# Kernel tuning notes

Hardware: AMD Instinct MI355X
Metric: run time of the kernel (lower is better)

Reference implementation:

```python
import jax, jax.numpy as jnp
import numpy as np

N_NODES = 50000
N_EDGES = 800000
IN_DIM = 256
HID = 64
HEADS = 4
N_CLASSES = 40
NEG_SLOPE = 0.2  # DGL GATConv default LeakyReLU slope


def setup_inputs() -> dict:
    key = jax.random.key(0)
    ks = jax.random.split(key, 8)
    features = jax.random.normal(ks[0], (N_NODES, IN_DIM), dtype=jnp.float32)
    src = jax.random.randint(ks[1], (N_EDGES,), 0, N_NODES, dtype=jnp.int32)
    dst = jax.random.randint(ks[2], (N_EDGES,), 0, N_NODES, dtype=jnp.int32)
    # GATConv params (Xavier-ish scale)
    W0 = jax.random.normal(ks[3], (IN_DIM, HEADS * HID), dtype=jnp.float32) / np.sqrt(IN_DIM)
    attn_l = jax.random.normal(ks[4], (HEADS, HID), dtype=jnp.float32) / np.sqrt(HID)
    attn_r = jax.random.normal(ks[5], (HEADS, HID), dtype=jnp.float32) / np.sqrt(HID)
    # Final FC layer
    fc_W = jax.random.normal(ks[6], (HEADS * HID, N_CLASSES), dtype=jnp.float32) / np.sqrt(HEADS * HID)
    fc_b = jax.random.normal(ks[7], (N_CLASSES,), dtype=jnp.float32) * 0.01
    return {"features": features, "W0": W0, "attn_l": attn_l, "attn_r": attn_r,
            "fc_W": fc_W, "fc_b": fc_b, "src": src, "dst": dst}


def _gat_conv(feat, W, a_l, a_r, src, dst):
    # feat: [N, F_in] -> projected [N, H, D]
    h = (feat @ W).reshape(feat.shape[0], HEADS, HID)
    el = jnp.einsum('nhd,hd->nh', h, a_l)  # [N, H]
    er = jnp.einsum('nhd,hd->nh', h, a_r)  # [N, H]
    e = el[src] + er[dst]                  # [E, H]
    e = jnp.where(e > 0, e, NEG_SLOPE * e)  # LeakyReLU
    # segment softmax over incoming edges of each destination node
    m = jax.ops.segment_max(e, dst, num_segments=N_NODES)  # [N, H]
    m = jnp.where(jnp.isfinite(m), m, 0.0)
    ex = jnp.exp(e - m[dst])
    s = jax.ops.segment_sum(ex, dst, num_segments=N_NODES)  # [N, H]
    alpha = ex / s[dst]                                      # [E, H]
    # weighted aggregation of source features
    msgs = alpha[:, :, None] * h[src]                        # [E, H, D]
    return jax.ops.segment_sum(msgs, dst, num_segments=N_NODES)  # [N, H, D]


def reference(features, W0, attn_l, attn_r, fc_W, fc_b, src, dst):
    h = _gat_conv(features, W0, attn_l, attn_r, src, dst)   # [N, H, D]
    h = jax.nn.relu(h).reshape(N_NODES, HEADS * HID)        # flatten(1)
    # dropout is identity in eval mode (training=False)
    return h @ fc_W + fc_b                                  # [N, num_classes]
```

## Files before the change

kernel.cpp:

```cpp
#include <hip/hip_runtime.h>

#define N_NODES 50000
#define N_EDGES 800000
#define IN_DIM 256
#define HID 64
#define HEADS 4
#define NFEAT 256
#define N_CLASSES 40
#define NC_PAD 48
#define NEG_SLOPE 0.2f
#define BIN_CAP 64

typedef __attribute__((ext_vector_type(8))) short short8;
typedef __attribute__((ext_vector_type(4))) float f32x4;

__device__ __forceinline__ unsigned short f2bf(float x) {
    unsigned u = __float_as_uint(x);
    unsigned r = u + 0x7FFFu + ((u >> 16) & 1u);
    return (unsigned short)(r >> 16);
}
__device__ __forceinline__ float bf2f(unsigned short u) {
    return __uint_as_float(((unsigned)u) << 16);
}
__device__ __forceinline__ float bf_lo(unsigned u) {
    return __uint_as_float(u << 16);
}
__device__ __forceinline__ float bf_hi(unsigned u) {
    return __uint_as_float(u & 0xFFFF0000u);
}

__global__ __launch_bounds__(256) void pack_weights(
    const float* __restrict__ W0, unsigned short* __restrict__ Wf,
    const float* __restrict__ W2, unsigned short* __restrict__ Wf2,
    int* __restrict__ cnt)
{
    int t = blockIdx.x * 256 + threadIdx.x;
    if (t < N_NODES) cnt[t] = 0;
    if (t < 65536) {
        int c = t & 255;
        int k = t >> 8;
        int kb = k >> 5, r = k & 31;
        int g = r >> 3, e = r & 7;
        Wf[((size_t)(kb * 256 + c) * 4 + g) * 8 + e] = f2bf(W0[(size_t)k * 256 + c]);
    } else {
        int t2 = t - 65536;
        if (t2 >= 8 * NC_PAD * 32) return;
        int c = (t2 >> 5) % NC_PAD;
        int kb = t2 / (NC_PAD * 32);
        int r = t2 & 31;
        int g = r >> 3, e = r & 7;
        int k = kb * 32 + g * 8 + e;
        float v = (c < N_CLASSES) ? W2[(size_t)k * N_CLASSES + c] : 0.f;
        Wf2[((size_t)(kb * NC_PAD + c) * 4 + g) * 8 + e] = f2bf(v);
    }
}

__global__ __launch_bounds__(256) void proj_mfma(
    const float* __restrict__ feat, const unsigned short* __restrict__ Wf,
    const float* __restrict__ al, const float* __restrict__ ar,
    unsigned short* __restrict__ hb16, float* __restrict__ el, float* __restrict__ er)
{
    const int tid  = threadIdx.x;
    const int lane = tid & 63;
    const int w    = tid >> 6;
    const int c    = lane & 15;
    const int g    = lane >> 4;
    const int row0 = blockIdx.x * 64;

    float alv[16], arv[16];
    #pragma unroll
    for (int f = 0; f < 16; ++f) { alv[f] = al[f * 16 + c]; arv[f] = ar[f * 16 + c]; }

    f32x4 acc[16];
    #pragma unroll
    for (int f = 0; f < 16; ++f) acc[f] = (f32x4){0.f, 0.f, 0.f, 0.f};

    const int arow = min(row0 + w * 16 + c, N_NODES - 1);
    const float* ap = &feat[(size_t)arow * IN_DIM + g * 8];

    for (int kb = 0; kb < 8; ++kb) {
        float4 v0 = *reinterpret_cast<const float4*>(ap + kb * 32);
        float4 v1 = *reinterpret_cast<const float4*>(ap + kb * 32 + 4);
        unsigned short us[8];
        us[0]=f2bf(v0.x); us[1]=f2bf(v0.y); us[2]=f2bf(v0.z); us[3]=f2bf(v0.w);
        us[4]=f2bf(v1.x); us[5]=f2bf(v1.y); us[6]=f2bf(v1.z); us[7]=f2bf(v1.w);
        short8 av = *reinterpret_cast<short8*>(us);
        #pragma unroll
        for (int f = 0; f < 16; ++f) {
            short8 bv = *reinterpret_cast<const short8*>(
                &Wf[((size_t)(kb * 256 + f * 16 + c) * 4 + g) * 8]);
            acc[f] = __builtin_amdgcn_mfma_f32_16x16x32_bf16(av, bv, acc[f], 0, 0, 0);
        }
    }

    const int baserow = row0 + w * 16 + g * 4;
    #pragma unroll
    for (int reg = 0; reg < 4; ++reg) {
        int grow = baserow + reg;
        bool ok = grow < N_NODES;
        float pl[4] = {0.f,0.f,0.f,0.f}, pr[4] = {0.f,0.f,0.f,0.f};
        #pragma unroll
        for (int f = 0; f < 16; ++f) {
            float v = acc[f][reg];
            pl[f >> 2] += v * alv[f];
            pr[f >> 2] += v * arv[f];
            if (ok) hb16[(size_t)grow * NFEAT + f * 16 + c] = f2bf(v);
        }
        #pragma unroll
        for (int hh = 0; hh < 4; ++hh) {
            #pragma unroll
            for (int off = 8; off; off >>= 1) {
                pl[hh] += __shfl_xor(pl[hh], off);
                pr[hh] += __shfl_xor(pr[hh], off);
            }
        }
        if (ok && c == 0) {
            #pragma unroll
            for (int hh = 0; hh < 4; ++hh) {
                el[grow * 4 + hh] = pl[hh];
                er[grow * 4 + hh] = pr[hh];
            }
        }
    }
}

__global__ __launch_bounds__(256) void fc_mfma(
    const unsigned short* __restrict__ aggb, const unsigned short* __restrict__ Wf2,
    const float* __restrict__ bias, float* __restrict__ out)
{
    const int tid  = threadIdx.x;
    const int lane = tid & 63;
    const int w    = tid >> 6;
    const int c    = lane & 15;
    const int g    = lane >> 4;
    const int row0 = blockIdx.x * 64;

    f32x4 acc[3];
    #pragma unroll
    for (int f = 0; f < 3; ++f) acc[f] = (f32x4){0.f, 0.f, 0.f, 0.f};

    const int arow = min(row0 + w * 16 + c, N_NODES - 1);
    const unsigned short* ap = &aggb[(size_t)arow * NFEAT + g * 8];

    for (int kb = 0; kb < 8; ++kb) {
        short8 av = *reinterpret_cast<const short8*>(ap + kb * 32);
        #pragma unroll
        for (int f = 0; f < 3; ++f) {
            short8 bv = *reinterpret_cast<const short8*>(
                &Wf2[((size_t)(kb * NC_PAD + f * 16 + c) * 4 + g) * 8]);
            acc[f] = __builtin_amdgcn_mfma_f32_16x16x32_bf16(av, bv, acc[f], 0, 0, 0);
        }
    }

    const int baserow = row0 + w * 16 + g * 4;
    #pragma unroll
    for (int reg = 0; reg < 4; ++reg) {
        int grow = baserow + reg;
        if (grow >= N_NODES) continue;
        #pragma unroll
        for (int f = 0; f < 3; ++f) {
            int col = f * 16 + c;
            if (col < N_CLASSES)
                out[(size_t)grow * N_CLASSES + col] = acc[f][reg] + bias[col];
        }
    }
}

__global__ __launch_bounds__(256) void scatter_bins(
    const int* __restrict__ src, const int* __restrict__ dst,
    int* __restrict__ cnt,
    const float4* __restrict__ el4, const float4* __restrict__ er4,
    uint4* __restrict__ bins)
{
    int e = blockIdx.x * 256 + threadIdx.x;
    if (e >= N_EDGES) return;
    int d = dst[e], s = src[e];
    int pos = atomicAdd(&cnt[d], 1);
    if (pos >= BIN_CAP) return;
    float4 l = el4[s];
    float4 r = er4[d];
    float t0 = l.x + r.x; t0 = t0 > 0.f ? t0 : NEG_SLOPE * t0;
    float t1 = l.y + r.y; t1 = t1 > 0.f ? t1 : NEG_SLOPE * t1;
    float t2 = l.z + r.z; t2 = t2 > 0.f ? t2 : NEG_SLOPE * t2;
    float t3 = l.w + r.w; t3 = t3 > 0.f ? t3 : NEG_SLOPE * t3;
    unsigned y = (unsigned)f2bf(__expf(t0)) | ((unsigned)f2bf(__expf(t1)) << 16);
    unsigned z = (unsigned)f2bf(__expf(t2)) | ((unsigned)f2bf(__expf(t3)) << 16);
    bins[(d << 6) + pos] = make_uint4((unsigned)s, y, z, 0u);
}

__global__ __launch_bounds__(256) void gat_agg_kernel(
    const int* __restrict__ cnt, const uint4* __restrict__ bins,
    const uint4* __restrict__ hb4, uint4* __restrict__ aggb4)
{
    const int lane  = threadIdx.x & 63;
    const int w     = threadIdx.x >> 6;
    const int d     = blockIdx.x * 4 + w;
    const int hlane = lane & 31;
    const int head  = hlane >> 3;
    const int ehalf = lane >> 5;
    const bool hi   = (head & 1) != 0;

    if (d >= N_NODES) return;
    const int deg = min(cnt[d], BIN_CAP);

    float acc[8] = {0.f,0.f,0.f,0.f,0.f,0.f,0.f,0.f};
    float sm = 0.f;
    const uint4* hp = hb4 + hlane;
    const uint4* bp = bins + (d << 6);

    #pragma unroll 4
    for (int jj = 0; jj < deg; jj += 2) {
        const int idx = jj + ehalf;
        const bool valid = idx < deg;
        uint4 entry = bp[min(idx, deg - 1)];
        unsigned ew = (head & 2) ? entry.z : entry.y;
        float ex = hi ? bf_hi(ew) : bf_lo(ew);
        ex = valid ? ex : 0.f;
        sm += ex;
        uint4 pv = hp[(size_t)entry.x * 32];
        acc[0] = fmaf(ex, bf_lo(pv.x), acc[0]);
        acc[1] = fmaf(ex, bf_hi(pv.x), acc[1]);
        acc[2] = fmaf(ex, bf_lo(pv.y), acc[2]);
        acc[3] = fmaf(ex, bf_hi(pv.y), acc[3]);
        acc[4] = fmaf(ex, bf_lo(pv.z), acc[4]);
        acc[5] = fmaf(ex, bf_hi(pv.z), acc[5]);
        acc[6] = fmaf(ex, bf_lo(pv.w), acc[6]);
        acc[7] = fmaf(ex, bf_hi(pv.w), acc[7]);
    }

    #pragma unroll
    for (int i = 0; i < 8; ++i) acc[i] += __shfl_xor(acc[i], 32);
    sm += __shfl_xor(sm, 32);

    const float inv = (deg > 0) ? 1.f / sm : 0.f;
    if (ehalf == 0) {
        uint4 r;
        r.x = (unsigned)f2bf(fmaxf(acc[0]*inv, 0.f)) | ((unsigned)f2bf(fmaxf(acc[1]*inv, 0.f)) << 16);
        r.y = (unsigned)f2bf(fmaxf(acc[2]*inv, 0.f)) | ((unsigned)f2bf(fmaxf(acc[3]*inv, 0.f)) << 16);
        r.z = (unsigned)f2bf(fmaxf(acc[4]*inv, 0.f)) | ((unsigned)f2bf(fmaxf(acc[5]*inv, 0.f)) << 16);
        r.w = (unsigned)f2bf(fmaxf(acc[6]*inv, 0.f)) | ((unsigned)f2bf(fmaxf(acc[7]*inv, 0.f)) << 16);
        aggb4[(d << 5) + hlane] = r;
    }
}

extern "C" void kernel_launch(void* const* d_in, const int* in_sizes, int n_in,
                              void* d_out, int out_size, void* d_ws, size_t ws_size,
                              hipStream_t stream)
{
    const float* features = (const float*)d_in[0];
    const float* W0       = (const float*)d_in[1];
    const float* attn_l   = (const float*)d_in[2];
    const float* attn_r   = (const float*)d_in[3];
    const float* fc_W     = (const float*)d_in[4];
    const float* fc_b     = (const float*)d_in[5];
    const int*   src      = (const int*)d_in[6];
    const int*   dst      = (const int*)d_in[7];
    float* out = (float*)d_out;

    char* ws = (char*)d_ws;
    unsigned short* hb16 = (unsigned short*)ws;
    ws += (size_t)N_NODES * NFEAT * sizeof(unsigned short);
    unsigned short* aggb = (unsigned short*)ws;
    ws += (size_t)N_NODES * NFEAT * sizeof(unsigned short);
    unsigned short* Wf = (unsigned short*)ws;
    ws += (size_t)IN_DIM * NFEAT * sizeof(unsigned short);
    unsigned short* Wf2 = (unsigned short*)ws;
    ws += (size_t)8 * NC_PAD * 32 * sizeof(unsigned short);
    float* el = (float*)ws;  ws += (size_t)N_NODES * HEADS * sizeof(float);
    float* er = (float*)ws;  ws += (size_t)N_NODES * HEADS * sizeof(float);
    int* cnt = (int*)ws;     ws += (size_t)N_NODES * sizeof(int);
    ws += (16 - ((size_t)ws & 15)) & 15;
    uint4* bins = (uint4*)ws;

    pack_weights<<<(65536 + 8 * NC_PAD * 32 + 255) / 256, 256, 0, stream>>>(
        W0, Wf, fc_W, Wf2, cnt);

    proj_mfma<<<(N_NODES + 63) / 64, 256, 0, stream>>>(
        features, Wf, attn_l, attn_r, hb16, el, er);

    scatter_bins<<<(N_EDGES + 255) / 256, 256, 0, stream>>>(
        src, dst, cnt, (const float4*)el, (const float4*)er, bins);

    gat_agg_kernel<<<(N_NODES + 3) / 4, 256, 0, stream>>>(
        cnt, bins, (const uint4*)hb16, (uint4*)aggb);

    fc_mfma<<<(N_NODES + 63) / 64, 256, 0, stream>>>(aggb, Wf2, fc_b, out);
}
```

Before: 165.1 us.

## Store only source index in bins and compute attention exp in aggregation

The scatter kernel now writes a 4-byte source index per bin slot instead of a 16-byte entry holding the source and precomputed bf16 exp scores. The aggregation kernel recomputes the LeakyReLU and exp per edge from el[src] and er[dst], which shrinks the bin write and read traffic and drops a bf16 rounding step. The trade is an extra gathered el load and an exp per lane per edge inside the aggregation loop. It also moves score computation from the edge-parallel stage into the node-parallel stage.

```diff
diff --git a/kernel.cpp b/kernel.cpp
--- a/kernel.cpp
+++ b/kernel.cpp
@@ -18,9 +18,6 @@
     unsigned u = __float_as_uint(x);
     unsigned r = u + 0x7FFFu + ((u >> 16) & 1u);
     return (unsigned short)(r >> 16);
-}
-__device__ __forceinline__ float bf2f(unsigned short u) {
-    return __uint_as_float(((unsigned)u) << 16);
 }
 __device__ __forceinline__ float bf_lo(unsigned u) {
     return __uint_as_float(u << 16);
@@ -168,28 +165,19 @@
 
 __global__ __launch_bounds__(256) void scatter_bins(
     const int* __restrict__ src, const int* __restrict__ dst,
-    int* __restrict__ cnt,
-    const float4* __restrict__ el4, const float4* __restrict__ er4,
-    uint4* __restrict__ bins)
+    int* __restrict__ cnt, int* __restrict__ bins_src)
 {
     int e = blockIdx.x * 256 + threadIdx.x;
     if (e >= N_EDGES) return;
-    int d = dst[e], s = src[e];
+    int d = dst[e];
     int pos = atomicAdd(&cnt[d], 1);
     if (pos >= BIN_CAP) return;
-    float4 l = el4[s];
-    float4 r = er4[d];
-    float t0 = l.x + r.x; t0 = t0 > 0.f ? t0 : NEG_SLOPE * t0;
-    float t1 = l.y + r.y; t1 = t1 > 0.f ? t1 : NEG_SLOPE * t1;
-    float t2 = l.z + r.z; t2 = t2 > 0.f ? t2 : NEG_SLOPE * t2;
-    float t3 = l.w + r.w; t3 = t3 > 0.f ? t3 : NEG_SLOPE * t3;
-    unsigned y = (unsigned)f2bf(__expf(t0)) | ((unsigned)f2bf(__expf(t1)) << 16);
-    unsigned z = (unsigned)f2bf(__expf(t2)) | ((unsigned)f2bf(__expf(t3)) << 16);
-    bins[(d << 6) + pos] = make_uint4((unsigned)s, y, z, 0u);
+    bins_src[(d << 6) + pos] = src[e];
 }
 
 __global__ __launch_bounds__(256) void gat_agg_kernel(
-    const int* __restrict__ cnt, const uint4* __restrict__ bins,
+    const int* __restrict__ cnt, const int* __restrict__ bins_src,
+    const float* __restrict__ el, const float* __restrict__ er,
     const uint4* __restrict__ hb4, uint4* __restrict__ aggb4)
 {
     const int lane  = threadIdx.x & 63;
@@ -198,26 +186,27 @@
     const int hlane = lane & 31;
     const int head  = hlane >> 3;
     const int ehalf = lane >> 5;
-    const bool hi   = (head & 1) != 0;
 
     if (d >= N_NODES) return;
     const int deg = min(cnt[d], BIN_CAP);
+    const float er_h = er[(d << 2) + head];
 
     float acc[8] = {0.f,0.f,0.f,0.f,0.f,0.f,0.f,0.f};
     float sm = 0.f;
     const uint4* hp = hb4 + hlane;
-    const uint4* bp = bins + (d << 6);
+    const int*   bp = bins_src + (d << 6);
 
     #pragma unroll 4
     for (int jj = 0; jj < deg; jj += 2) {
         const int idx = jj + ehalf;
         const bool valid = idx < deg;
-        uint4 entry = bp[min(idx, deg - 1)];
-        unsigned ew = (head & 2) ? entry.z : entry.y;
-        float ex = hi ? bf_hi(ew) : bf_lo(ew);
+        const int s = bp[min(idx, deg - 1)];
+        float e = el[(s << 2) + head] + er_h;
+        e = e > 0.f ? e : NEG_SLOPE * e;
+        float ex = __expf(e);
         ex = valid ? ex : 0.f;
         sm += ex;
-        uint4 pv = hp[(size_t)entry.x * 32];
+        uint4 pv = hp[(size_t)s * 32];
         acc[0] = fmaf(ex, bf_lo(pv.x), acc[0]);
         acc[1] = fmaf(ex, bf_hi(pv.x), acc[1]);
         acc[2] = fmaf(ex, bf_lo(pv.y), acc[2]);
@@ -269,8 +258,7 @@
     float* el = (float*)ws;  ws += (size_t)N_NODES * HEADS * sizeof(float);
     float* er = (float*)ws;  ws += (size_t)N_NODES * HEADS * sizeof(float);
     int* cnt = (int*)ws;     ws += (size_t)N_NODES * sizeof(int);
-    ws += (16 - ((size_t)ws & 15)) & 15;
-    uint4* bins = (uint4*)ws;
+    int* bins_src = (int*)ws;
 
     pack_weights<<<(65536 + 8 * NC_PAD * 32 + 255) / 256, 256, 0, stream>>>(
         W0, Wf, fc_W, Wf2, cnt);
@@ -279,10 +267,10 @@
         features, Wf, attn_l, attn_r, hb16, el, er);
 
     scatter_bins<<<(N_EDGES + 255) / 256, 256, 0, stream>>>(
-        src, dst, cnt, (const float4*)el, (const float4*)er, bins);
+        src, dst, cnt, bins_src);
 
     gat_agg_kernel<<<(N_NODES + 3) / 4, 256, 0, stream>>>(
-        cnt, bins, (const uint4*)hb16, (uint4*)aggb);
+        cnt, bins_src, el, er, (const uint4*)hb16, (uint4*)aggb);
 
     fc_mfma<<<(N_NODES + 63) / 64, 256, 0, stream>>>(aggb, Wf2, fc_b, out);
 }
```

Measured after the change: 175.7 us. +6.4%, slower.

## Fuse GAT aggregation with final FC layer via shared-memory tile

Applied to the files above, without the earlier changes.

Merges the aggregation kernel and the FC MFMA kernel into one. Each block now aggregates 16 destination nodes, with each wave handling 4 of them, and writes the bf16 ReLU outputs to LDS. Three waves then apply the 256x40 FC layer with MFMA. This removes the global write and re-read of the 25.6MB aggregated feature buffer and one kernel launch. In exchange each block runs fewer concurrent nodes per wave, which may reduce latency hiding in the gather loop, and the fourth wave sits idle during the FC step.

```diff
diff --git a/kernel.cpp b/kernel.cpp
--- a/kernel.cpp
+++ b/kernel.cpp
@@ -18,9 +18,6 @@
     unsigned u = __float_as_uint(x);
     unsigned r = u + 0x7FFFu + ((u >> 16) & 1u);
     return (unsigned short)(r >> 16);
-}
-__device__ __forceinline__ float bf2f(unsigned short u) {
-    return __uint_as_float(((unsigned)u) << 16);
 }
 __device__ __forceinline__ float bf_lo(unsigned u) {
     return __uint_as_float(u << 16);
@@ -124,48 +121,6 @@
     }
 }
 
-__global__ __launch_bounds__(256) void fc_mfma(
-    const unsigned short* __restrict__ aggb, const unsigned short* __restrict__ Wf2,
-    const float* __restrict__ bias, float* __restrict__ out)
-{
-    const int tid  = threadIdx.x;
-    const int lane = tid & 63;
-    const int w    = tid >> 6;
-    const int c    = lane & 15;
-    const int g    = lane >> 4;
-    const int row0 = blockIdx.x * 64;
-
-    f32x4 acc[3];
-    #pragma unroll
-    for (int f = 0; f < 3; ++f) acc[f] = (f32x4){0.f, 0.f, 0.f, 0.f};
-
-    const int arow = min(row0 + w * 16 + c, N_NODES - 1);
-    const unsigned short* ap = &aggb[(size_t)arow * NFEAT + g * 8];
-
-    for (int kb = 0; kb < 8; ++kb) {
-        short8 av = *reinterpret_cast<const short8*>(ap + kb * 32);
-        #pragma unroll
-        for (int f = 0; f < 3; ++f) {
-            short8 bv = *reinterpret_cast<const short8*>(
-                &Wf2[((size_t)(kb * NC_PAD + f * 16 + c) * 4 + g) * 8]);
-            acc[f] = __builtin_amdgcn_mfma_f32_16x16x32_bf16(av, bv, acc[f], 0, 0, 0);
-        }
-    }
-
-    const int baserow = row0 + w * 16 + g * 4;
-    #pragma unroll
-    for (int reg = 0; reg < 4; ++reg) {
-        int grow = baserow + reg;
-        if (grow >= N_NODES) continue;
-        #pragma unroll
-        for (int f = 0; f < 3; ++f) {
-            int col = f * 16 + c;
-            if (col < N_CLASSES)
-                out[(size_t)grow * N_CLASSES + col] = acc[f][reg] + bias[col];
-        }
-    }
-}
-
 __global__ __launch_bounds__(256) void scatter_bins(
     const int* __restrict__ src, const int* __restrict__ dst,
     int* __restrict__ cnt,
@@ -188,58 +143,84 @@
     bins[(d << 6) + pos] = make_uint4((unsigned)s, y, z, 0u);
 }
 
-__global__ __launch_bounds__(256) void gat_agg_kernel(
+__global__ __launch_bounds__(256) void gat_agg_fc_kernel(
     const int* __restrict__ cnt, const uint4* __restrict__ bins,
-    const uint4* __restrict__ hb4, uint4* __restrict__ aggb4)
-{
+    const uint4* __restrict__ hb4, const unsigned short* __restrict__ Wf2,
+    const float* __restrict__ bias, float* __restrict__ out)
+{
+    __shared__ unsigned short lds_agg[16][264];
     const int lane  = threadIdx.x & 63;
     const int w     = threadIdx.x >> 6;
-    const int d     = blockIdx.x * 4 + w;
     const int hlane = lane & 31;
     const int head  = hlane >> 3;
     const int ehalf = lane >> 5;
     const bool hi   = (head & 1) != 0;
-
-    if (d >= N_NODES) return;
-    const int deg = min(cnt[d], BIN_CAP);
-
-    float acc[8] = {0.f,0.f,0.f,0.f,0.f,0.f,0.f,0.f};
-    float sm = 0.f;
-    const uint4* hp = hb4 + hlane;
-    const uint4* bp = bins + (d << 6);
-
-    #pragma unroll 4
-    for (int jj = 0; jj < deg; jj += 2) {
-        const int idx = jj + ehalf;
-        const bool valid = idx < deg;
-        uint4 entry = bp[min(idx, deg - 1)];
-        unsigned ew = (head & 2) ? entry.z : entry.y;
-        float ex = hi ? bf_hi(ew) : bf_lo(ew);
-        ex = valid ? ex : 0.f;
-        sm += ex;
-        uint4 pv = hp[(size_t)entry.x * 32];
-        acc[0] = fmaf(ex, bf_lo(pv.x), acc[0]);
-        acc[1] = fmaf(ex, bf_hi(pv.x), acc[1]);
-        acc[2] = fmaf(ex, bf_lo(pv.y), acc[2]);
-        acc[3] = fmaf(ex, bf_hi(pv.y), acc[3]);
-        acc[4] = fmaf(ex, bf_lo(pv.z), acc[4]);
-        acc[5] = fmaf(ex, bf_hi(pv.z), acc[5]);
-        acc[6] = fmaf(ex, bf_lo(pv.w), acc[6]);
-        acc[7] = fmaf(ex, bf_hi(pv.w), acc[7]);
-    }
-
-    #pragma unroll
-    for (int i = 0; i < 8; ++i) acc[i] += __shfl_xor(acc[i], 32);
-    sm += __shfl_xor(sm, 32);
-
-    const float inv = (deg > 0) ? 1.f / sm : 0.f;
-    if (ehalf == 0) {
-        uint4 r;
-        r.x = (unsigned)f2bf(fmaxf(acc[0]*inv, 0.f)) | ((unsigned)f2bf(fmaxf(acc[1]*inv, 0.f)) << 16);
-        r.y = (unsigned)f2bf(fmaxf(acc[2]*inv, 0.f)) | ((unsigned)f2bf(fmaxf(acc[3]*inv, 0.f)) << 16);
-        r.z = (unsigned)f2bf(fmaxf(acc[4]*inv, 0.f)) | ((unsigned)f2bf(fmaxf(acc[5]*inv, 0.f)) << 16);
-        r.w = (unsigned)f2bf(fmaxf(acc[6]*inv, 0.f)) | ((unsigned)f2bf(fmaxf(acc[7]*inv, 0.f)) << 16);
-        aggb4[(d << 5) + hlane] = r;
+    const int nbase = blockIdx.x * 16;
+
+    for (int t = 0; t < 4; ++t) {
+        const int d   = nbase + w * 4 + t;
+        const int deg = min(cnt[d], BIN_CAP);
+
+        float acc[8] = {0.f,0.f,0.f,0.f,0.f,0.f,0.f,0.f};
+        float sm = 0.f;
+        const uint4* hp = hb4 + hlane;
+        const uint4* bp = bins + (d << 6);
+
+        #pragma unroll 4
+        for (int jj = 0; jj < deg; jj += 2) {
+            const int idx = jj + ehalf;
+            const bool valid = idx < deg;
+            uint4 entry = bp[min(idx, deg - 1)];
+            unsigned ew = (head & 2) ? entry.z : entry.y;
+            float ex = hi ? bf_hi(ew) : bf_lo(ew);
+            ex = valid ? ex : 0.f;
+            sm += ex;
+            uint4 pv = hp[(size_t)entry.x * 32];
+            acc[0] = fmaf(ex, bf_lo(pv.x), acc[0]);
+            acc[1] = fmaf(ex, bf_hi(pv.x), acc[1]);
+            acc[2] = fmaf(ex, bf_lo(pv.y), acc[2]);
+            acc[3] = fmaf(ex, bf_hi(pv.y), acc[3]);
+            acc[4] = fmaf(ex, bf_lo(pv.z), acc[4]);
+            acc[5] = fmaf(ex, bf_hi(pv.z), acc[5]);
+            acc[6] = fmaf(ex, bf_lo(pv.w), acc[6]);
+            acc[7] = fmaf(ex, bf_hi(pv.w), acc[7]);
+        }
+
+        #pragma unroll
+        for (int i = 0; i < 8; ++i) acc[i] += __shfl_xor(acc[i], 32);
+        sm += __shfl_xor(sm, 32);
+
+        const float inv = (deg > 0) ? 1.f / sm : 0.f;
+        if (ehalf == 0) {
+            unsigned short us[8];
+            #pragma unroll
+            for (int i = 0; i < 8; ++i) us[i] = f2bf(fmaxf(acc[i] * inv, 0.f));
+            *reinterpret_cast<uint4*>(&lds_agg[w * 4 + t][hlane * 8]) =
+                *reinterpret_cast<uint4*>(us);
+        }
+    }
+
+    __syncthreads();
+
+    if (w < 3) {
+        const int c = lane & 15;
+        const int g = lane >> 4;
+        f32x4 facc = (f32x4){0.f, 0.f, 0.f, 0.f};
+        #pragma unroll
+        for (int kb = 0; kb < 8; ++kb) {
+            short8 av = *reinterpret_cast<const short8*>(&lds_agg[c][kb * 32 + g * 8]);
+            short8 bv = *reinterpret_cast<const short8*>(
+                &Wf2[((size_t)(kb * NC_PAD + w * 16 + c) * 4 + g) * 8]);
+            facc = __builtin_amdgcn_mfma_f32_16x16x32_bf16(av, bv, facc, 0, 0, 0);
+        }
+        const int col = w * 16 + c;
+        if (col < N_CLASSES) {
+            const float b = bias[col];
+            #pragma unroll
+            for (int reg = 0; reg < 4; ++reg) {
+                out[(size_t)(nbase + g * 4 + reg) * N_CLASSES + col] = facc[reg] + b;
+            }
+        }
     }
 }
 
@@ -259,8 +240,6 @@
 
     char* ws = (char*)d_ws;
     unsigned short* hb16 = (unsigned short*)ws;
-    ws += (size_t)N_NODES * NFEAT * sizeof(unsigned short);
-    unsigned short* aggb = (unsigned short*)ws;
     ws += (size_t)N_NODES * NFEAT * sizeof(unsigned short);
     unsigned short* Wf = (unsigned short*)ws;
     ws += (size_t)IN_DIM * NFEAT * sizeof(unsigned short);
@@ -281,8 +260,6 @@
     scatter_bins<<<(N_EDGES + 255) / 256, 256, 0, stream>>>(
         src, dst, cnt, (const float4*)el, (const float4*)er, bins);
 
-    gat_agg_kernel<<<(N_NODES + 3) / 4, 256, 0, stream>>>(
-        cnt, bins, (const uint4*)hb16, (uint4*)aggb);
-
-    fc_mfma<<<(N_NODES + 63) / 64, 256, 0, stream>>>(aggb, Wf2, fc_b, out);
-}
+    gat_agg_fc_kernel<<<N_NODES / 16, 256, 0, stream>>>(
+        cnt, bins, (const uint4*)hb16, Wf2, fc_b, out);
+}
```

New measurement: 155.1 us (median of 3 runs). 6.1% less time.
